# Optimization experiments

Measured on AMD Instinct MI355X. Metric: run time of the kernel, lower is better.

## Reference

```python
import jax, jax.numpy as jnp
import numpy as np

N, K, D = 32768, 8192, 512

def setup_inputs() -> dict:
    key = jax.random.key(0)
    kx, kw = jax.random.split(key)
    x = jax.random.normal(kx, (N, D), dtype=jnp.float32)
    # nn.Embedding weight init: uniform(-1/K, 1/K)
    codebook = jax.random.uniform(kw, (K, D), dtype=jnp.float32, minval=-1.0 / K, maxval=1.0 / K)
    return {"x": x, "codebook": codebook}

def reference(x, codebook):
    distances = (
        jnp.sum(x * x, axis=1, keepdims=True)
        + jnp.sum(codebook * codebook, axis=1)
        - 2.0 * jnp.einsum("nd,kd->nk", x, codebook)
    )
    encoding_indices = jnp.argmin(distances, axis=1)            # [N]
    encodings = jax.nn.one_hot(encoding_indices, K, dtype=x.dtype)  # [N, K]
    quantized = jnp.einsum("nk,kd->nd", encodings, codebook)    # [N, D]
    return quantized, encodings, encoding_indices
```

## Files before the change

### kernel.cpp

```cpp
#include <hip/hip_runtime.h>
#include <stdint.h>

#define D     512
#define BM    128
#define BN    128
#define BK    128
#define CAND  48
#define MARGIN 5e-4f
#define KDIM  8192

typedef __attribute__((ext_vector_type(4))) float f32x4;
typedef __attribute__((ext_vector_type(8))) short s16x8;

__device__ __forceinline__ short f2bf(float f) {
  unsigned u = __float_as_uint(f);
  u = (u + 0x7FFFu + ((u >> 16) & 1u)) >> 16;
  return (short)u;
}

__device__ __forceinline__ s16x8 pack_bf8(float4 a, float4 b) {
  s16x8 v;
  v[0] = f2bf(a.x); v[1] = f2bf(a.y); v[2] = f2bf(a.z); v[3] = f2bf(a.w);
  v[4] = f2bf(b.x); v[5] = f2bf(b.y); v[6] = f2bf(b.z); v[7] = f2bf(b.w);
  return v;
}

__device__ __forceinline__ unsigned fkey(float f) {
  unsigned u = __float_as_uint(f);
  return (u >> 31) ? ~u : (u | 0x80000000u);
}
__device__ __forceinline__ float unfkey(unsigned k) {
  unsigned u = (k >> 31) ? (k & 0x7FFFFFFFu) : ~k;
  return __uint_as_float(u);
}

__global__ __launch_bounds__(256) void vq_prep(const float* __restrict__ cb,
                                               unsigned short* __restrict__ wh,
                                               float* __restrict__ b32, int K) {
  int wid  = blockIdx.x * 4 + (threadIdx.x >> 6);
  int lane = threadIdx.x & 63;
  if (wid >= K) return;
  const float* row = cb + (size_t)wid * D + lane * 8;
  float4 a = *(const float4*)row;
  float4 b = *(const float4*)(row + 4);
  float v[8] = {a.x, a.y, a.z, a.w, b.x, b.y, b.z, b.w};
  double s = 0.0;
#pragma unroll
  for (int j = 0; j < 8; ++j) { float sq = v[j] * v[j]; s += (double)sq; }
  s16x8 p = pack_bf8(a, b);
  *(s16x8*)((short*)wh + (size_t)wid * D + lane * 8) = p;
#pragma unroll
  for (int m = 1; m < 64; m <<= 1) s += __shfl_xor(s, m);
  if (lane == 0) b32[wid] = (float)s;
}

__device__ __forceinline__ void stage4(const unsigned short* __restrict__ wh,
                                       short (*wb)[BN * BK], int kt2, int c2,
                                       int w, int lane) {
#pragma unroll
  for (int i = 0; i < 4; ++i) {
    const int sb  = (w * 4 + i) * 64;
    const int s   = sb + lane;
    const int row = s >> 4;
    const int sir = s & 15;
    const int ksl = sir ^ (row & 15);
    const unsigned short* src = wh + (size_t)(kt2 * BN + row) * D + c2 * BK + ksl * 8;
    short* dst = &wb[c2][sb * 8];
    __builtin_amdgcn_global_load_lds(
        (const __attribute__((address_space(1))) unsigned int*)src,
        (__attribute__((address_space(3))) unsigned int*)dst, 16, 0, 0);
  }
}

__global__ __launch_bounds__(512, 2) void vq_main(
    const float* __restrict__ x, const float* __restrict__ cb,
    const unsigned short* __restrict__ wh, const float* __restrict__ b32g,
    float* __restrict__ out_q, float* __restrict__ out_enc, float* __restrict__ out_idx,
    int N, int K) {
  __shared__ short wb[4][BN * BK];
  __shared__ unsigned rowmin[BM];
  __shared__ unsigned rowcnt[BM];
  __shared__ unsigned candb[BM][CAND];

  const int t    = threadIdx.x;
  const int lane = t & 63;
  const int w    = t >> 6;
  const int wr   = w >> 1;
  const int wc   = w & 1;
  const int l15  = lane & 15;
  const int l16  = lane >> 4;
  const int m_base = blockIdx.x * BM;
  const int nkt  = K / BN;
  float* const enc_blk = out_enc + (size_t)m_base * K;

  if (t < BM) { rowmin[t] = 0xFFFFFFFFu; rowcnt[t] = 0u; }

  stage4(wh, wb, 0, 0, w, lane);
  stage4(wh, wb, 0, 1, w, lane);

  s16x8 afr[2][16];
#pragma unroll
  for (int mi = 0; mi < 2; ++mi) {
    const float* xr = x + (size_t)(m_base + 32 * wr + 16 * mi + l15) * D;
#pragma unroll
    for (int f = 0; f < 16; ++f) {
      const float* p = xr + (f * 4 + l16) * 8;
      float4 a = *(const float4*)p;
      float4 b = *(const float4*)(p + 4);
      afr[mi][f] = pack_bf8(a, b);
    }
  }
  __syncthreads();

  for (int kt = 0; kt < nkt; ++kt) {
    float b32v[4];
#pragma unroll
    for (int ni = 0; ni < 4; ++ni)
      b32v[ni] = b32g[kt * BN + 64 * wc + 16 * ni + l15];

    f32x4 acc[2][4];
#pragma unroll
    for (int mi = 0; mi < 2; ++mi)
#pragma unroll
      for (int ni = 0; ni < 4; ++ni) acc[mi][ni] = (f32x4){0.f, 0.f, 0.f, 0.f};

#pragma unroll
    for (int c = 0; c < 4; ++c) {
      {
        const f32x4 z4 = {0.f, 0.f, 0.f, 0.f};
        f32x4* ez = (f32x4*)(enc_blk + (size_t)kt * (BM * KDIM / 64));
        __builtin_nontemporal_store(z4, ez + (c * 2 + 0) * 512 + t);
        __builtin_nontemporal_store(z4, ez + (c * 2 + 1) * 512 + t);
      }
      const int kt2 = kt + ((c + 2) >> 2);
      if (kt2 < nkt) stage4(wh, wb, kt2, (c + 2) & 3, w, lane);

      const short* wp = &wb[c][0];
      __builtin_amdgcn_s_setprio(1);
#pragma unroll
      for (int ks = 0; ks < 4; ++ks) {
        s16x8 bfr[4];
#pragma unroll
        for (int ni = 0; ni < 4; ++ni) {
          const int row = 64 * wc + 16 * ni + l15;
          const int sl  = (ks * 4 + l16) ^ (row & 15);
          bfr[ni] = *(const s16x8*)(wp + row * BK + sl * 8);
        }
#pragma unroll
        for (int mi = 0; mi < 2; ++mi)
#pragma unroll
          for (int ni = 0; ni < 4; ++ni)
            acc[mi][ni] = __builtin_amdgcn_mfma_f32_16x16x32_bf16(
                afr[mi][c * 4 + ks], bfr[ni], acc[mi][ni], 0, 0, 0);
      }
      __builtin_amdgcn_s_setprio(0);
      if (kt2 < nkt) asm volatile("s_waitcnt vmcnt(4)" ::: "memory");
      else           asm volatile("s_waitcnt vmcnt(0)" ::: "memory");
      __builtin_amdgcn_sched_barrier(0);
      __builtin_amdgcn_s_barrier();
    }

    float tv[2][4][4];
#pragma unroll
    for (int mi = 0; mi < 2; ++mi)
#pragma unroll
      for (int ni = 0; ni < 4; ++ni)
#pragma unroll
        for (int r = 0; r < 4; ++r)
          tv[mi][ni][r] = fmaf(-2.0f, acc[mi][ni][r], b32v[ni]);

    if (kt == 0) {
#pragma unroll
      for (int mi = 0; mi < 2; ++mi)
#pragma unroll
        for (int r = 0; r < 4; ++r) {
          float m = fminf(fminf(tv[mi][0][r], tv[mi][1][r]),
                          fminf(tv[mi][2][r], tv[mi][3][r]));
          atomicMin(&rowmin[32 * wr + 16 * mi + 4 * l16 + r], fkey(m));
        }
      __syncthreads();
    }

#pragma unroll
    for (int mi = 0; mi < 2; ++mi) {
      const int rbase = 32 * wr + 16 * mi + 4 * l16;
      const uint4 ru = *(const uint4*)&rowmin[rbase];
      const unsigned rua[4] = {ru.x, ru.y, ru.z, ru.w};
#pragma unroll
      for (int r = 0; r < 4; ++r) {
        const float rm  = unfkey(rua[r]);
        const float thr = rm + MARGIN;
        const float mn  = fminf(fminf(tv[mi][0][r], tv[mi][1][r]),
                                fminf(tv[mi][2][r], tv[mi][3][r]));
        if (mn < rm) atomicMin(&rowmin[rbase + r], fkey(mn));
#pragma unroll
        for (int ni = 0; ni < 4; ++ni) {
          if (tv[mi][ni][r] <= thr) {
            unsigned p = atomicAdd(&rowcnt[rbase + r], 1u);
            if (p < CAND) candb[rbase + r][p] = (unsigned)(kt * BN + 64 * wc + 16 * ni + l15);
          }
        }
      }
    }
  }
  __syncthreads();

  for (int r = w; r < BM; r += 8) {
    const int n = m_base + r;
    const float* xr = x + (size_t)n * D + lane * 8;
    float4 xa = *(const float4*)xr;
    float4 xb = *(const float4*)(xr + 4);
    float xv[8] = {xa.x, xa.y, xa.z, xa.w, xb.x, xb.y, xb.z, xb.w};
    double s = 0.0;
#pragma unroll
    for (int j = 0; j < 8; ++j) { float sq = xv[j] * xv[j]; s += (double)sq; }
#pragma unroll
    for (int m = 1; m < 64; m <<= 1) s += __shfl_xor(s, m);
    const float Arow = (float)s;

    const unsigned c = rowcnt[r];
    const bool uselist = (c >= 1u && c <= (unsigned)CAND);
    const int nc = uselist ? (int)c : K;
    unsigned long long best = 0xFFFFFFFFFFFFFFFFull;
    for (int i = 0; i < nc; ++i) {
      const int k = uselist ? (int)candb[r][i] : i;
      const float* wp = cb + (size_t)k * D + lane * 8;
      float4 wa = *(const float4*)wp;
      float4 wbv = *(const float4*)(wp + 4);
      float wv[8] = {wa.x, wa.y, wa.z, wa.w, wbv.x, wbv.y, wbv.z, wbv.w};
      double d = 0.0;
#pragma unroll
      for (int j = 0; j < 8; ++j) d += (double)xv[j] * (double)wv[j];
#pragma unroll
      for (int m = 1; m < 64; m <<= 1) d += __shfl_xor(d, m);
      const float C32 = (float)d;
      const float T1  = Arow + b32g[k];
      const float sc  = T1 - 2.0f * C32;
      unsigned long long pk = ((unsigned long long)__float_as_uint(sc) << 32) | (unsigned)k;
      best = best < pk ? best : pk;
    }
    const int kstar = (int)(best & 0xFFFFFFFFu);

    if (lane == 0) {
      out_idx[n] = (float)kstar;
      out_enc[(size_t)n * K + kstar] = 1.0f;
    }
    const float* qs = cb + (size_t)kstar * D + lane * 8;
    float4 q0 = *(const float4*)qs;
    float4 q1 = *(const float4*)(qs + 4);
    f32x4* qd = (f32x4*)(out_q + (size_t)n * D + lane * 8);
    f32x4 q0v = {q0.x, q0.y, q0.z, q0.w};
    f32x4 q1v = {q1.x, q1.y, q1.z, q1.w};
    __builtin_nontemporal_store(q0v, qd);
    __builtin_nontemporal_store(q1v, qd + 1);
  }
}

extern "C" void kernel_launch(void* const* d_in, const int* in_sizes, int n_in,
                              void* d_out, int out_size, void* d_ws, size_t ws_size,
                              hipStream_t stream) {
  const float* x  = (const float*)d_in[0];
  const float* cb = (const float*)d_in[1];
  const int N = in_sizes[0] / D;
  const int K = in_sizes[1] / D;

  unsigned short* wh = (unsigned short*)d_ws;
  float* b32 = (float*)((char*)d_ws + (size_t)K * D * sizeof(unsigned short));

  float* out     = (float*)d_out;
  float* out_q   = out;
  float* out_enc = out + (size_t)N * D;
  float* out_idx = out + (size_t)N * D + (size_t)N * K;

  vq_prep<<<(K + 3) / 4, 256, 0, stream>>>(cb, wh, b32, K);
  vq_main<<<N / BM, 512, 0, stream>>>(x, cb, wh, b32, out_q, out_enc, out_idx, N, K);
}
```

Baseline: 463.4 us.

## Switch distance GEMM from bf16 to fp8 MFMA with scaled codebook

Quantizes x and the codebook (pre-scaled by 8192) to fp8 e4m3 and uses the 16x16x32 fp8 MFMA instead of bf16, which halves the codebook bytes staged into LDS and the shared-memory read traffic. The LDS swizzle and staging are reworked for 8-bit elements, and the norm bias is scaled to match. The candidate margin and candidate buffer size are enlarged so that exact rescoring can still find the true argmin despite the coarser fp8 scores. The fixed 8192 scale assumes codebook magnitudes near 1/K, and fp8 precision on x may let the true minimum fall outside the margin.

```diff
diff --git a/kernel.cpp b/kernel.cpp
--- a/kernel.cpp
+++ b/kernel.cpp
@@ -1,28 +1,21 @@
 #include <hip/hip_runtime.h>
+#include <hip/hip_fp8.h>
 #include <stdint.h>
 
 #define D     512
 #define BM    128
 #define BN    128
-#define BK    128
-#define CAND  48
-#define MARGIN 5e-4f
+#define BKC   128
+#define CAND  96
+#define MARGIN 7e-4f
+#define MARGINS (8192.0f * MARGIN)
 #define KDIM  8192
 
 typedef __attribute__((ext_vector_type(4))) float f32x4;
-typedef __attribute__((ext_vector_type(8))) short s16x8;
-
-__device__ __forceinline__ short f2bf(float f) {
-  unsigned u = __float_as_uint(f);
-  u = (u + 0x7FFFu + ((u >> 16) & 1u)) >> 16;
-  return (short)u;
-}
-
-__device__ __forceinline__ s16x8 pack_bf8(float4 a, float4 b) {
-  s16x8 v;
-  v[0] = f2bf(a.x); v[1] = f2bf(a.y); v[2] = f2bf(a.z); v[3] = f2bf(a.w);
-  v[4] = f2bf(b.x); v[5] = f2bf(b.y); v[6] = f2bf(b.z); v[7] = f2bf(b.w);
-  return v;
+
+__device__ __forceinline__ unsigned char f2fp8(float f) {
+  __hip_fp8_e4m3 q(f);
+  return (unsigned char)q.__x;
 }
 
 __device__ __forceinline__ unsigned fkey(float f) {
@@ -35,7 +28,7 @@
 }
 
 __global__ __launch_bounds__(256) void vq_prep(const float* __restrict__ cb,
-                                               unsigned short* __restrict__ wh,
+                                               unsigned char* __restrict__ w8,
                                                float* __restrict__ b32, int K) {
   int wid  = blockIdx.x * 4 + (threadIdx.x >> 6);
   int lane = threadIdx.x & 63;
@@ -45,27 +38,30 @@
   float4 b = *(const float4*)(row + 4);
   float v[8] = {a.x, a.y, a.z, a.w, b.x, b.y, b.z, b.w};
   double s = 0.0;
-#pragma unroll
-  for (int j = 0; j < 8; ++j) { float sq = v[j] * v[j]; s += (double)sq; }
-  s16x8 p = pack_bf8(a, b);
-  *(s16x8*)((short*)wh + (size_t)wid * D + lane * 8) = p;
+  unsigned long long p = 0ull;
+#pragma unroll
+  for (int j = 0; j < 8; ++j) {
+    float sq = v[j] * v[j]; s += (double)sq;
+    p |= (unsigned long long)f2fp8(v[j] * 8192.0f) << (8 * j);
+  }
+  *(unsigned long long*)(w8 + (size_t)wid * D + lane * 8) = p;
 #pragma unroll
   for (int m = 1; m < 64; m <<= 1) s += __shfl_xor(s, m);
   if (lane == 0) b32[wid] = (float)s;
 }
 
-__device__ __forceinline__ void stage4(const unsigned short* __restrict__ wh,
-                                       short (*wb)[BN * BK], int kt2, int c2,
+__device__ __forceinline__ void stage2(const unsigned char* __restrict__ w8,
+                                       unsigned char (*wb)[BN * BKC], int kt2, int c2,
                                        int w, int lane) {
 #pragma unroll
-  for (int i = 0; i < 4; ++i) {
-    const int sb  = (w * 4 + i) * 64;
+  for (int i = 0; i < 2; ++i) {
+    const int sb  = (w * 2 + i) * 64;
     const int s   = sb + lane;
-    const int row = s >> 4;
-    const int sir = s & 15;
-    const int ksl = sir ^ (row & 15);
-    const unsigned short* src = wh + (size_t)(kt2 * BN + row) * D + c2 * BK + ksl * 8;
-    short* dst = &wb[c2][sb * 8];
+    const int row = s >> 3;
+    const int j   = s & 7;
+    const int k16 = j ^ (row & 7);
+    const unsigned char* src = w8 + (size_t)(kt2 * BN + row) * D + c2 * BKC + k16 * 16;
+    unsigned char* dst = &wb[c2][sb * 16];
     __builtin_amdgcn_global_load_lds(
         (const __attribute__((address_space(1))) unsigned int*)src,
         (__attribute__((address_space(3))) unsigned int*)dst, 16, 0, 0);
@@ -74,10 +70,10 @@
 
 __global__ __launch_bounds__(512, 2) void vq_main(
     const float* __restrict__ x, const float* __restrict__ cb,
-    const unsigned short* __restrict__ wh, const float* __restrict__ b32g,
+    const unsigned char* __restrict__ w8, const float* __restrict__ b32g,
     float* __restrict__ out_q, float* __restrict__ out_enc, float* __restrict__ out_idx,
     int N, int K) {
-  __shared__ short wb[4][BN * BK];
+  __shared__ unsigned char wb[4][BN * BKC];
   __shared__ unsigned rowmin[BM];
   __shared__ unsigned rowcnt[BM];
   __shared__ unsigned candb[BM][CAND];
@@ -95,19 +91,23 @@
 
   if (t < BM) { rowmin[t] = 0xFFFFFFFFu; rowcnt[t] = 0u; }
 
-  stage4(wh, wb, 0, 0, w, lane);
-  stage4(wh, wb, 0, 1, w, lane);
-
-  s16x8 afr[2][16];
+  stage2(w8, wb, 0, 0, w, lane);
+  stage2(w8, wb, 0, 1, w, lane);
+
+  long afr[2][16];
 #pragma unroll
   for (int mi = 0; mi < 2; ++mi) {
     const float* xr = x + (size_t)(m_base + 32 * wr + 16 * mi + l15) * D;
 #pragma unroll
     for (int f = 0; f < 16; ++f) {
-      const float* p = xr + (f * 4 + l16) * 8;
+      const float* p = xr + f * 32 + l16 * 8;
       float4 a = *(const float4*)p;
       float4 b = *(const float4*)(p + 4);
-      afr[mi][f] = pack_bf8(a, b);
+      float v[8] = {a.x, a.y, a.z, a.w, b.x, b.y, b.z, b.w};
+      unsigned long long pk = 0ull;
+#pragma unroll
+      for (int j = 0; j < 8; ++j) pk |= (unsigned long long)f2fp8(v[j]) << (8 * j);
+      afr[mi][f] = (long)pk;
     }
   }
   __syncthreads();
@@ -116,7 +116,7 @@
     float b32v[4];
 #pragma unroll
     for (int ni = 0; ni < 4; ++ni)
-      b32v[ni] = b32g[kt * BN + 64 * wc + 16 * ni + l15];
+      b32v[ni] = 8192.0f * b32g[kt * BN + 64 * wc + 16 * ni + l15];
 
     f32x4 acc[2][4];
 #pragma unroll
@@ -126,31 +126,31 @@
 
 #pragma unroll
     for (int c = 0; c < 4; ++c) {
+      const int kt2 = kt + ((c + 2) >> 2);
+      if (kt2 < nkt) stage2(w8, wb, kt2, (c + 2) & 3, w, lane);
       {
         const f32x4 z4 = {0.f, 0.f, 0.f, 0.f};
         f32x4* ez = (f32x4*)(enc_blk + (size_t)kt * (BM * KDIM / 64));
         __builtin_nontemporal_store(z4, ez + (c * 2 + 0) * 512 + t);
         __builtin_nontemporal_store(z4, ez + (c * 2 + 1) * 512 + t);
       }
-      const int kt2 = kt + ((c + 2) >> 2);
-      if (kt2 < nkt) stage4(wh, wb, kt2, (c + 2) & 3, w, lane);
-
-      const short* wp = &wb[c][0];
+
+      const unsigned char* wp = &wb[c][0];
       __builtin_amdgcn_s_setprio(1);
 #pragma unroll
       for (int ks = 0; ks < 4; ++ks) {
-        s16x8 bfr[4];
+        long bfr[4];
 #pragma unroll
         for (int ni = 0; ni < 4; ++ni) {
-          const int row = 64 * wc + 16 * ni + l15;
-          const int sl  = (ks * 4 + l16) ^ (row & 15);
-          bfr[ni] = *(const s16x8*)(wp + row * BK + sl * 8);
+          const int row  = 64 * wc + 16 * ni + l15;
+          const int slot = (ks * 2 + (l16 >> 1)) ^ (row & 7);
+          bfr[ni] = *(const long*)(wp + row * BKC + slot * 16 + (l16 & 1) * 8);
         }
 #pragma unroll
         for (int mi = 0; mi < 2; ++mi)
 #pragma unroll
           for (int ni = 0; ni < 4; ++ni)
-            acc[mi][ni] = __builtin_amdgcn_mfma_f32_16x16x32_bf16(
+            acc[mi][ni] = __builtin_amdgcn_mfma_f32_16x16x32_fp8_fp8(
                 afr[mi][c * 4 + ks], bfr[ni], acc[mi][ni], 0, 0, 0);
       }
       __builtin_amdgcn_s_setprio(0);
@@ -189,7 +189,7 @@
 #pragma unroll
       for (int r = 0; r < 4; ++r) {
         const float rm  = unfkey(rua[r]);
-        const float thr = rm + MARGIN;
+        const float thr = rm + MARGINS;
         const float mn  = fminf(fminf(tv[mi][0][r], tv[mi][1][r]),
                                 fminf(tv[mi][2][r], tv[mi][3][r]));
         if (mn < rm) atomicMin(&rowmin[rbase + r], fkey(mn));
@@ -264,14 +264,14 @@
   const int N = in_sizes[0] / D;
   const int K = in_sizes[1] / D;
 
-  unsigned short* wh = (unsigned short*)d_ws;
-  float* b32 = (float*)((char*)d_ws + (size_t)K * D * sizeof(unsigned short));
+  unsigned char* w8 = (unsigned char*)d_ws;
+  float* b32 = (float*)((char*)d_ws + (size_t)K * D);
 
   float* out     = (float*)d_out;
   float* out_q   = out;
   float* out_enc = out + (size_t)N * D;
   float* out_idx = out + (size_t)N * D + (size_t)N * K;
 
-  vq_prep<<<(K + 3) / 4, 256, 0, stream>>>(cb, wh, b32, K);
-  vq_main<<<N / BM, 512, 0, stream>>>(x, cb, wh, b32, out_q, out_enc, out_idx, N, K);
-}
+  vq_prep<<<(K + 3) / 4, 256, 0, stream>>>(cb, w8, b32, K);
+  vq_main<<<N / BM, 512, 0, stream>>>(x, cb, w8, b32, out_q, out_enc, out_idx, N, K);
+}
```

Measured after the change: 502.1 us. 1.08x slower.
